# Optimization experiments

Measured on AMD Instinct MI355X. Metric: run time of the kernel, lower is better.

## Reference

```python
import jax, jax.numpy as jnp
import numpy as np

N_NODES = 30000
N_EDGES = 480000
N_GRAPHS = 64
NEG_SLOPE = 0.2
BN_EPS = 1e-5


def _leaky_relu(x, slope=NEG_SLOPE):
    return jnp.where(x >= 0, x, slope * x)


def gat_layer(x, src, dst, W, att_src, att_dst, bias, heads, ch, n_nodes):
    # x: [N, F_in]; W: [F_in, heads*ch]
    h = (x @ W).reshape(n_nodes, heads, ch)            # [N,H,C]
    a_s = jnp.sum(h * att_src, axis=-1)                # [N,H]
    a_d = jnp.sum(h * att_dst, axis=-1)                # [N,H]
    e = _leaky_relu(a_s[src] + a_d[dst])               # [E,H] per-edge logits
    # edge-softmax over incoming edges of each destination node
    m = jax.ops.segment_max(e, dst, num_segments=n_nodes)   # [N,H]
    ex = jnp.exp(e - m[dst])
    denom = jax.ops.segment_sum(ex, dst, num_segments=n_nodes)
    alpha = ex / denom[dst]                            # [E,H]
    msg = alpha[:, :, None] * h[src]                   # [E,H,C]
    out = jax.ops.segment_sum(msg, dst, num_segments=n_nodes)  # [N,H,C]
    return out.reshape(n_nodes, heads * ch) + bias


def setup_inputs() -> dict:
    key = jax.random.key(0)
    ks = jax.random.split(key, 16)
    x = jax.random.normal(ks[0], (N_NODES, 3), dtype=jnp.float32)
    edge_index = jax.random.randint(ks[1], (2, N_EDGES), 0, N_NODES, dtype=jnp.int64)
    batch = jnp.sort(jax.random.randint(ks[2], (N_NODES,), 0, N_GRAPHS, dtype=jnp.int64))

    def glorot(k, shape):
        fan = shape[0] + shape[-1]
        s = jnp.sqrt(6.0 / fan)
        return jax.random.uniform(k, shape, jnp.float32, -s, s)

    params = dict(
        W1=glorot(ks[3], (3, 8 * 64)),
        att_src1=glorot(ks[4], (8, 64)) * 0.1,
        att_dst1=glorot(ks[5], (8, 64)) * 0.1,
        b1=jnp.zeros((8 * 64,), jnp.float32),
        W2=glorot(ks[6], (8 * 64, 4 * 32)),
        att_src2=glorot(ks[7], (4, 32)) * 0.1,
        att_dst2=glorot(ks[8], (4, 32)) * 0.1,
        b2=jnp.zeros((4 * 32,), jnp.float32),
        Wfc=glorot(ks[9], (4 * 32, 32)),
        bfc=jnp.zeros((32,), jnp.float32),
        bn_gamma=jnp.ones((32,), jnp.float32),
        bn_beta=jnp.zeros((32,), jnp.float32),
        Wheat=glorot(ks[10], (32, 3)),
        bheat=jnp.zeros((3,), jnp.float32),
        Wdehyd=glorot(ks[11], (32, 2)),
        bdehyd=jnp.zeros((2,), jnp.float32),
    )
    return {"x": x, "edge_index": edge_index, "batch": batch, **params}


def reference(x, edge_index, batch, W1, att_src1, att_dst1, b1,
              W2, att_src2, att_dst2, b2, Wfc, bfc, bn_gamma, bn_beta,
              Wheat, bheat, Wdehyd, bdehyd):
    n = x.shape[0]
    # GATConv adds self-loops by default
    loops = jnp.arange(n, dtype=edge_index.dtype)
    src = jnp.concatenate([edge_index[0], loops])
    dst = jnp.concatenate([edge_index[1], loops])

    x1 = jax.nn.relu(gat_layer(x, src, dst, W1, att_src1, att_dst1, b1, 8, 64, n))   # [N,512]
    x2 = jax.nn.relu(gat_layer(x1, src, dst, W2, att_src2, att_dst2, b2, 4, 32, n))  # [N,128]
    h = x1[:, : x2.shape[1]] + x2                                                    # [N,128]

    # global_mean_pool over graph ids
    sums = jax.ops.segment_sum(h, batch, num_segments=N_GRAPHS)                      # [G,128]
    cnts = jax.ops.segment_sum(jnp.ones((n,), h.dtype), batch, num_segments=N_GRAPHS)
    pooled = sums / jnp.maximum(cnts, 1.0)[:, None]

    z = pooled @ Wfc + bfc                                                           # [G,32]
    mu = jnp.mean(z, axis=0)
    var = jnp.var(z, axis=0)
    z = bn_gamma * (z - mu) / jnp.sqrt(var + BN_EPS) + bn_beta
    z = jax.nn.relu(z)
    return (z @ Wheat + bheat, z @ Wdehyd + bdehyd)
```

## Files before the change

### kernel.cpp

```cpp
#include <hip/hip_runtime.h>
#include <math.h>


#define N_NODES 30000
#define N_GRAPHS 64

__global__ __launch_bounds__(256) void k_att1(
    const float* __restrict__ x, const float* __restrict__ W1,
    const float* __restrict__ asw, const float* __restrict__ adw,
    float* __restrict__ a_s, float* __restrict__ a_d, int n)
{
    __shared__ float Ps[24], Pd[24];
    int t = threadIdx.x;
    if (t < 48) {
        int which = t / 24;
        int idx = t - which * 24;
        int d = idx >> 3, h = idx & 7;
        const float* av = (which ? adw : asw) + h * 64;
        const float* wr = W1 + d * 512 + h * 64;
        float s = 0.f;
        #pragma unroll 8
        for (int c = 0; c < 64; ++c) s = fmaf(wr[c], av[c], s);
        (which ? Pd : Ps)[idx] = s;
    }
    __syncthreads();
    int node = blockIdx.x * 256 + t;
    if (node >= n) return;
    float x0 = x[node * 3 + 0];
    float x1v = x[node * 3 + 1];
    float x2v = x[node * 3 + 2];
    #pragma unroll
    for (int h = 0; h < 8; ++h) {
        a_s[node * 8 + h] = fmaf(x0, Ps[h], fmaf(x1v, Ps[8 + h], x2v * Ps[16 + h]));
        a_d[node * 8 + h] = fmaf(x0, Pd[h], fmaf(x1v, Pd[8 + h], x2v * Pd[16 + h]));
    }
}

__global__ void k_deg(const int* __restrict__ ei, int* __restrict__ deg,
                      int E0, int n)
{
    int e = blockIdx.x * blockDim.x + threadIdx.x;
    int Et = E0 + n;
    if (e >= Et) return;
    int dst = (e < E0) ? ei[E0 + e] : (e - E0);
    atomicAdd(&deg[dst], 1);
}

__global__ __launch_bounds__(1024) void k_scan(
    const int* __restrict__ deg, int* __restrict__ rowstart,
    int* __restrict__ cursor, int n)
{
    __shared__ int wsum[16];
    __shared__ int woff[17];
    __shared__ int carry_s;
    int tid = threadIdx.x, lane = tid & 63, wid = tid >> 6;
    if (tid == 0) carry_s = 0;
    __syncthreads();
    int nchunks = (n + 1023) >> 10;
    for (int c = 0; c < nchunks; ++c) {
        int i = (c << 10) + tid;
        int v = (i < n) ? deg[i] : 0;
        int s = v;
        #pragma unroll
        for (int off = 1; off < 64; off <<= 1) {
            int t = __shfl_up(s, off);
            if (lane >= off) s += t;
        }
        if (lane == 63) wsum[wid] = s;
        __syncthreads();
        if (wid == 0) {
            int ws = (lane < 16) ? wsum[lane] : 0;
            #pragma unroll
            for (int off = 1; off < 16; off <<= 1) {
                int t = __shfl_up(ws, off);
                if (lane >= off) ws += t;
            }
            if (lane < 16) woff[lane + 1] = ws;
            if (lane == 0) woff[0] = 0;
        }
        __syncthreads();
        int excl = carry_s + woff[wid] + s - v;
        if (i < n) { rowstart[i] = excl; cursor[i] = excl; }
        __syncthreads();
        if (tid == 0) carry_s += woff[16];
        __syncthreads();
    }
    if (tid == 0) rowstart[n] = carry_s;
}

__global__ void k_fill(const int* __restrict__ ei, int* __restrict__ cursor,
                       int* __restrict__ csr, int E0, int n)
{
    int e = blockIdx.x * blockDim.x + threadIdx.x;
    int Et = E0 + n;
    if (e >= Et) return;
    int src, dst;
    if (e < E0) { src = ei[e]; dst = ei[E0 + e]; }
    else        { src = e - E0; dst = e - E0; }
    int pos = atomicAdd(&cursor[dst], 1);
    csr[pos] = src;
}

__global__ __launch_bounds__(256) void k_gat1(
    const float* __restrict__ x, const float* __restrict__ W1,
    const float* __restrict__ a_s, const float* __restrict__ a_d,
    const int* __restrict__ rowstart, const int* __restrict__ csr,
    const float* __restrict__ bias, float* __restrict__ x1, int n)
{
    int lane = threadIdx.x & 63;
    int node = blockIdx.x * 4 + (threadIdx.x >> 6);
    if (node >= n) return;
    int rs = rowstart[node], re = rowstart[node + 1];
    int hd = lane >> 3;
    int slot = lane & 7;
    float adn = a_d[node * 8 + hd];

    float m = -1e30f, ssum = 0.f, S0 = 0.f, S1 = 0.f, S2 = 0.f;
    for (int i = rs + slot; i < re; i += 8) {
        int src = csr[i];
        float e = a_s[src * 8 + hd] + adn;
        e = (e >= 0.f) ? e : 0.2f * e;
        float x0 = x[src * 3 + 0];
        float x1v = x[src * 3 + 1];
        float x2v = x[src * 3 + 2];
        float mn = fmaxf(m, e);
        float sc = __expf(m - mn);
        float wgt = __expf(e - mn);
        ssum = fmaf(ssum, sc, wgt);
        S0 = fmaf(S0, sc, wgt * x0);
        S1 = fmaf(S1, sc, wgt * x1v);
        S2 = fmaf(S2, sc, wgt * x2v);
        m = mn;
    }
    #pragma unroll
    for (int off = 1; off < 8; off <<= 1) {
        float mo = __shfl_xor(m, off);
        float so = __shfl_xor(ssum, off);
        float t0 = __shfl_xor(S0, off);
        float t1 = __shfl_xor(S1, off);
        float t2 = __shfl_xor(S2, off);
        float mn = fmaxf(m, mo);
        float scA = __expf(m - mn);
        float scB = __expf(mo - mn);
        ssum = ssum * scA + so * scB;
        S0 = S0 * scA + t0 * scB;
        S1 = S1 * scA + t1 * scB;
        S2 = S2 * scA + t2 * scB;
        m = mn;
    }
    float inv = 1.f / ssum;
    S0 *= inv; S1 *= inv; S2 *= inv;

    const float4* w0p = (const float4*)(W1 + lane * 8);
    const float4* w1p = (const float4*)(W1 + 512 + lane * 8);
    const float4* w2p = (const float4*)(W1 + 1024 + lane * 8);
    const float4* bp  = (const float4*)(bias + lane * 8);
    float4* xp = (float4*)(x1 + (size_t)node * 512 + lane * 8);
    #pragma unroll
    for (int q = 0; q < 2; ++q) {
        float4 w0 = w0p[q], w1 = w1p[q], w2 = w2p[q], b = bp[q];
        float4 o;
        o.x = fmaxf(fmaf(S0, w0.x, fmaf(S1, w1.x, fmaf(S2, w2.x, b.x))), 0.f);
        o.y = fmaxf(fmaf(S0, w0.y, fmaf(S1, w1.y, fmaf(S2, w2.y, b.y))), 0.f);
        o.z = fmaxf(fmaf(S0, w0.z, fmaf(S1, w1.z, fmaf(S2, w2.z, b.z))), 0.f);
        o.w = fmaxf(fmaf(S0, w0.w, fmaf(S1, w1.w, fmaf(S2, w2.w, b.w))), 0.f);
        xp[q] = o;
    }
}

#define BM2 32
__global__ __launch_bounds__(256) void k_gemm2(
    const float* __restrict__ x1, const float* __restrict__ W2,
    const float* __restrict__ asw, const float* __restrict__ adw,
    float* __restrict__ h2, float* __restrict__ a_s2, float* __restrict__ a_d2,
    int n)
{
    int tid = threadIdx.x;
    int tr = tid >> 5;
    int tc = tid & 31;
    int bm = blockIdx.x * BM2;

    float acc[4][4];
    #pragma unroll
    for (int r = 0; r < 4; ++r)
        #pragma unroll
        for (int c = 0; c < 4; ++c) acc[r][c] = 0.f;

    const float* arow[4];
    #pragma unroll
    for (int r = 0; r < 4; ++r) {
        int row = bm + tr * 4 + r;
        row = row < n ? row : (n - 1);
        arow[r] = x1 + (size_t)row * 512;
    }
    const float* bcol = W2 + tc * 4;

    for (int k = 0; k < 512; k += 4) {
        float a_[4][4];
        #pragma unroll
        for (int r = 0; r < 4; ++r) {
            float4 av = *(const float4*)(arow[r] + k);
            a_[r][0] = av.x; a_[r][1] = av.y; a_[r][2] = av.z; a_[r][3] = av.w;
        }
        float b_[4][4];
        #pragma unroll
        for (int kk = 0; kk < 4; ++kk) {
            float4 bv = *(const float4*)(bcol + (size_t)(k + kk) * 128);
            b_[kk][0] = bv.x; b_[kk][1] = bv.y; b_[kk][2] = bv.z; b_[kk][3] = bv.w;
        }
        #pragma unroll
        for (int kk = 0; kk < 4; ++kk)
            #pragma unroll
            for (int r = 0; r < 4; ++r)
                #pragma unroll
                for (int c = 0; c < 4; ++c)
                    acc[r][c] = fmaf(a_[r][kk], b_[kk][c], acc[r][c]);
    }

    #pragma unroll
    for (int r = 0; r < 4; ++r) {
        int row = bm + tr * 4 + r;
        if (row < n) {
            float4 o;
            o.x = acc[r][0]; o.y = acc[r][1]; o.z = acc[r][2]; o.w = acc[r][3];
            *(float4*)(h2 + (size_t)row * 128 + tc * 4) = o;
        }
    }

    float4 ws = *(const float4*)(asw + tc * 4);
    float4 wd = *(const float4*)(adw + tc * 4);
    float ps[4], pd[4];
    #pragma unroll
    for (int r = 0; r < 4; ++r) {
        ps[r] = acc[r][0] * ws.x + acc[r][1] * ws.y + acc[r][2] * ws.z + acc[r][3] * ws.w;
        pd[r] = acc[r][0] * wd.x + acc[r][1] * wd.y + acc[r][2] * wd.z + acc[r][3] * wd.w;
    }
    #pragma unroll
    for (int off = 1; off < 8; off <<= 1) {
        #pragma unroll
        for (int r = 0; r < 4; ++r) {
            ps[r] += __shfl_xor(ps[r], off);
            pd[r] += __shfl_xor(pd[r], off);
        }
    }
    if ((tc & 7) == 0) {
        int hd = tc >> 3;
        #pragma unroll
        for (int r = 0; r < 4; ++r) {
            int row = bm + tr * 4 + r;
            if (row < n) {
                a_s2[row * 4 + hd] = ps[r];
                a_d2[row * 4 + hd] = pd[r];
            }
        }
    }
}

__global__ __launch_bounds__(256) void k_gat2(
    const float* __restrict__ h2, const float* __restrict__ a_s,
    const float* __restrict__ a_d, const int* __restrict__ rowstart,
    const int* __restrict__ csr, const float* __restrict__ bias,
    const float* __restrict__ x1, float* __restrict__ hres, int n)
{
    int lane = threadIdx.x & 63;
    int node = blockIdx.x * 4 + (threadIdx.x >> 6);
    if (node >= n) return;
    int rs = rowstart[node], re = rowstart[node + 1];
    int hd = lane >> 4;
    float adn = a_d[node * 4 + hd];

    float m = -1e30f, ssum = 0.f, acc0 = 0.f, acc1 = 0.f;
    int src_next = (rs < re) ? csr[rs] : 0;
    for (int i = rs; i < re; ++i) {
        int src = src_next;
        if (i + 1 < re) src_next = csr[i + 1];
        float e = a_s[src * 4 + hd] + adn;
        e = (e >= 0.f) ? e : 0.2f * e;
        float2 hv = *(const float2*)(h2 + (size_t)src * 128 + lane * 2);
        float mn = fmaxf(m, e);
        float sc = __expf(m - mn);
        float wgt = __expf(e - mn);
        ssum = fmaf(ssum, sc, wgt);
        acc0 = fmaf(acc0, sc, wgt * hv.x);
        acc1 = fmaf(acc1, sc, wgt * hv.y);
        m = mn;
    }
    float inv = 1.f / ssum;
    float2 xv = *(const float2*)(x1 + (size_t)node * 512 + lane * 2);
    float2 o;
    o.x = xv.x + fmaxf(fmaf(acc0, inv, bias[lane * 2 + 0]), 0.f);
    o.y = xv.y + fmaxf(fmaf(acc1, inv, bias[lane * 2 + 1]), 0.f);
    *(float2*)(hres + (size_t)node * 128 + lane * 2) = o;
}

__global__ __launch_bounds__(128) void k_pool(
    const float* __restrict__ hres, const int* __restrict__ batch,
    float* __restrict__ pooled, float* __restrict__ cnt, int n)
{
    int j = threadIdx.x;
    int n0 = blockIdx.x * 128;
    if (n0 >= n) return;
    int n1 = min(n0 + 128, n);
    int g = batch[n0];
    float acc = 0.f;
    int run = 0;
    for (int node = n0; node < n1; ++node) {
        int gb = batch[node];
        if (gb != g) {
            atomicAdd(&pooled[g * 128 + j], acc);
            if (j == 0) atomicAdd(&cnt[g], (float)run);
            acc = 0.f; run = 0; g = gb;
        }
        acc += hres[(size_t)node * 128 + j];
        run++;
    }
    atomicAdd(&pooled[g * 128 + j], acc);
    if (j == 0) atomicAdd(&cnt[g], (float)run);
}

__global__ __launch_bounds__(1024) void k_head(
    const float* __restrict__ pooled, const float* __restrict__ cnt,
    const float* __restrict__ Wfc, const float* __restrict__ bfc,
    const float* __restrict__ gamma, const float* __restrict__ beta,
    const float* __restrict__ Wheat, const float* __restrict__ bheat,
    const float* __restrict__ Wdehyd, const float* __restrict__ bdehyd,
    float* __restrict__ out)
{
    __shared__ float z[N_GRAPHS * 32];
    __shared__ float mu_s[32], rstd_s[32];
    int t = threadIdx.x;
    for (int idx = t; idx < N_GRAPHS * 32; idx += 1024) {
        int g = idx >> 5, j = idx & 31;
        float c = cnt[g];
        c = c < 1.f ? 1.f : c;
        float s = 0.f;
        for (int k = 0; k < 128; ++k)
            s = fmaf(pooled[g * 128 + k], Wfc[k * 32 + j], s);
        z[idx] = s / c + bfc[j];
    }
    __syncthreads();
    if (t < 32) {
        float mu = 0.f;
        for (int g = 0; g < N_GRAPHS; ++g) mu += z[g * 32 + t];
        mu *= (1.f / N_GRAPHS);
        float var = 0.f;
        for (int g = 0; g < N_GRAPHS; ++g) {
            float d = z[g * 32 + t] - mu;
            var = fmaf(d, d, var);
        }
        var *= (1.f / N_GRAPHS);
        mu_s[t] = mu;
        rstd_s[t] = 1.f / sqrtf(var + 1e-5f);
    }
    __syncthreads();
    for (int idx = t; idx < N_GRAPHS * 32; idx += 1024) {
        int j = idx & 31;
        float v = gamma[j] * (z[idx] - mu_s[j]) * rstd_s[j] + beta[j];
        z[idx] = v > 0.f ? v : 0.f;
    }
    __syncthreads();
    if (t < N_GRAPHS * 3) {
        int g = t / 3, r = t - g * 3;
        float s = 0.f;
        for (int j2 = 0; j2 < 32; ++j2)
            s = fmaf(z[g * 32 + j2], Wheat[j2 * 3 + r], s);
        out[t] = s + bheat[r];
    } else if (t < N_GRAPHS * 3 + N_GRAPHS * 2) {
        int idx = t - N_GRAPHS * 3;
        int g = idx >> 1, r = idx & 1;
        float s = 0.f;
        for (int j2 = 0; j2 < 32; ++j2)
            s = fmaf(z[g * 32 + j2], Wdehyd[j2 * 2 + r], s);
        out[N_GRAPHS * 3 + idx] = s + bdehyd[r];
    }
}

extern "C" void kernel_launch(void* const* d_in, const int* in_sizes, int n_in,
                              void* d_out, int out_size, void* d_ws, size_t ws_size,
                              hipStream_t stream)
{
    const float* x      = (const float*)d_in[0];
    const int*   ei     = (const int*)d_in[1];
    const int*   batch  = (const int*)d_in[2];
    const float* W1     = (const float*)d_in[3];
    const float* as1w   = (const float*)d_in[4];
    const float* ad1w   = (const float*)d_in[5];
    const float* b1     = (const float*)d_in[6];
    const float* W2     = (const float*)d_in[7];
    const float* as2w   = (const float*)d_in[8];
    const float* ad2w   = (const float*)d_in[9];
    const float* b2     = (const float*)d_in[10];
    const float* Wfc    = (const float*)d_in[11];
    const float* bfc    = (const float*)d_in[12];
    const float* gamma  = (const float*)d_in[13];
    const float* beta   = (const float*)d_in[14];
    const float* Wheat  = (const float*)d_in[15];
    const float* bheat  = (const float*)d_in[16];
    const float* Wdehyd = (const float*)d_in[17];
    const float* bdehyd = (const float*)d_in[18];
    float* out = (float*)d_out;

    const int N = N_NODES;
    const int E0 = in_sizes[1] / 2;
    const int Et = E0 + N;
    const int G = N_GRAPHS;

    char* w = (char*)d_ws;
    auto alloc = [&](size_t bytes) -> char* {
        char* p = w;
        w += (bytes + 255) & ~(size_t)255;
        return p;
    };
    float* x1    = (float*)alloc((size_t)N * 512 * 4);
    float* h2    = (float*)alloc((size_t)N * 128 * 4);
    float* hres  = (float*)alloc((size_t)N * 128 * 4);
    float* a_s1  = (float*)alloc((size_t)N * 8 * 4);
    float* a_d1  = (float*)alloc((size_t)N * 8 * 4);
    float* a_s2  = (float*)alloc((size_t)N * 4 * 4);
    float* a_d2  = (float*)alloc((size_t)N * 4 * 4);
    int* deg     = (int*)alloc((size_t)(N + 1) * 4);
    int* rowstart= (int*)alloc((size_t)(N + 1) * 4);
    int* cursor  = (int*)alloc((size_t)N * 4);
    int* csr     = (int*)alloc((size_t)Et * 4);
    float* pooled= (float*)alloc((size_t)G * 128 * 4);
    float* cntf  = (float*)alloc((size_t)G * 4);

    hipMemsetAsync(deg, 0, (size_t)(N + 1) * 4, stream);
    hipMemsetAsync(pooled, 0, (size_t)G * 128 * 4, stream);
    hipMemsetAsync(cntf, 0, (size_t)G * 4, stream);

    k_att1<<<(N + 255) / 256, 256, 0, stream>>>(x, W1, as1w, ad1w, a_s1, a_d1, N);
    k_deg<<<(Et + 255) / 256, 256, 0, stream>>>(ei, deg, E0, N);
    k_scan<<<1, 1024, 0, stream>>>(deg, rowstart, cursor, N);
    k_fill<<<(Et + 255) / 256, 256, 0, stream>>>(ei, cursor, csr, E0, N);
    k_gat1<<<(N + 3) / 4, 256, 0, stream>>>(x, W1, a_s1, a_d1, rowstart, csr, b1, x1, N);
    k_gemm2<<<(N + BM2 - 1) / BM2, 256, 0, stream>>>(x1, W2, as2w, ad2w, h2, a_s2, a_d2, N);
    k_gat2<<<(N + 3) / 4, 256, 0, stream>>>(h2, a_s2, a_d2, rowstart, csr, b2, x1, hres, N);
    k_pool<<<(N + 127) / 128, 128, 0, stream>>>(hres, batch, pooled, cntf, N);
    k_head<<<1, 1024, 0, stream>>>(pooled, cntf, Wfc, bfc, gamma, beta,
                                   Wheat, bheat, Wdehyd, bdehyd, out);
}
```

Measured before the change: 438.7 us.

## Tile layer-2 GEMM through double-buffered shared memory with larger per-thread blocks

The layer-2 projection GEMM, which used to read A and B straight from global memory per thread, now stages 64x32 A tiles (stored transposed and padded) and 32x128 W2 tiles in double-buffered LDS, prefetching the next tile into registers while computing. Each thread now computes a 4x8 output block instead of 4x4, and the attention-dot reductions are adjusted to the new column mapping. This is meant to cut redundant global/L2 traffic and raise arithmetic intensity, at the cost of more LDS use and registers, which can lower occupancy.

```diff
diff --git a/kernel.cpp b/kernel.cpp
--- a/kernel.cpp
+++ b/kernel.cpp
@@ -168,89 +168,164 @@
     }
 }
 
-#define BM2 32
+#define GM_BM 64
+#define GM_BK 32
+#define GM_APAD 68
 __global__ __launch_bounds__(256) void k_gemm2(
     const float* __restrict__ x1, const float* __restrict__ W2,
     const float* __restrict__ asw, const float* __restrict__ adw,
     float* __restrict__ h2, float* __restrict__ a_s2, float* __restrict__ a_d2,
     int n)
 {
+    __shared__ float As[2][GM_BK][GM_APAD];
+    __shared__ float Bs[2][GM_BK][128];
     int tid = threadIdx.x;
-    int tr = tid >> 5;
-    int tc = tid & 31;
-    int bm = blockIdx.x * BM2;
-
-    float acc[4][4];
+    int tr = tid >> 4;
+    int tc = tid & 15;
+    int bm = blockIdx.x * GM_BM;
+
+    int aRow0 = tid >> 3;
+    int aC40  = tid & 7;
+    int aRow1 = (tid + 256) >> 3;
+    int aC41  = (tid + 256) & 7;
+    float4 aReg0, aReg1, bReg[4];
+
+    int arowg0 = bm + aRow0; arowg0 = arowg0 < n ? arowg0 : (n - 1);
+    int arowg1 = bm + aRow1; arowg1 = arowg1 < n ? arowg1 : (n - 1);
+    const float* aPtr0 = x1 + (size_t)arowg0 * 512 + aC40 * 4;
+    const float* aPtr1 = x1 + (size_t)arowg1 * 512 + aC41 * 4;
+
+    float acc[4][8];
     #pragma unroll
     for (int r = 0; r < 4; ++r)
         #pragma unroll
-        for (int c = 0; c < 4; ++c) acc[r][c] = 0.f;
-
-    const float* arow[4];
-    #pragma unroll
-    for (int r = 0; r < 4; ++r) {
-        int row = bm + tr * 4 + r;
-        row = row < n ? row : (n - 1);
-        arow[r] = x1 + (size_t)row * 512;
-    }
-    const float* bcol = W2 + tc * 4;
-
-    for (int k = 0; k < 512; k += 4) {
-        float a_[4][4];
+        for (int c = 0; c < 8; ++c) acc[r][c] = 0.f;
+
+    {
+        aReg0 = *(const float4*)(aPtr0);
+        aReg1 = *(const float4*)(aPtr1);
         #pragma unroll
-        for (int r = 0; r < 4; ++r) {
-            float4 av = *(const float4*)(arow[r] + k);
-            a_[r][0] = av.x; a_[r][1] = av.y; a_[r][2] = av.z; a_[r][3] = av.w;
-        }
-        float b_[4][4];
+        for (int j = 0; j < 4; ++j) {
+            int li = tid + j * 256;
+            bReg[j] = *(const float4*)(W2 + (size_t)(li >> 5) * 128 + (li & 31) * 4);
+        }
+        As[0][aC40 * 4 + 0][aRow0] = aReg0.x;
+        As[0][aC40 * 4 + 1][aRow0] = aReg0.y;
+        As[0][aC40 * 4 + 2][aRow0] = aReg0.z;
+        As[0][aC40 * 4 + 3][aRow0] = aReg0.w;
+        As[0][aC41 * 4 + 0][aRow1] = aReg1.x;
+        As[0][aC41 * 4 + 1][aRow1] = aReg1.y;
+        As[0][aC41 * 4 + 2][aRow1] = aReg1.z;
+        As[0][aC41 * 4 + 3][aRow1] = aReg1.w;
         #pragma unroll
-        for (int kk = 0; kk < 4; ++kk) {
-            float4 bv = *(const float4*)(bcol + (size_t)(k + kk) * 128);
-            b_[kk][0] = bv.x; b_[kk][1] = bv.y; b_[kk][2] = bv.z; b_[kk][3] = bv.w;
+        for (int j = 0; j < 4; ++j) {
+            int li = tid + j * 256;
+            *(float4*)(&Bs[0][li >> 5][(li & 31) * 4]) = bReg[j];
+        }
+    }
+    __syncthreads();
+
+    for (int s = 0; s < 16; ++s) {
+        int buf = s & 1;
+        if (s < 15) {
+            int k0 = (s + 1) * GM_BK;
+            aReg0 = *(const float4*)(aPtr0 + k0);
+            aReg1 = *(const float4*)(aPtr1 + k0);
+            #pragma unroll
+            for (int j = 0; j < 4; ++j) {
+                int li = tid + j * 256;
+                bReg[j] = *(const float4*)(W2 + (size_t)(k0 + (li >> 5)) * 128 + (li & 31) * 4);
+            }
         }
         #pragma unroll
-        for (int kk = 0; kk < 4; ++kk)
+        for (int kk = 0; kk < GM_BK; ++kk) {
+            float4 a4 = *(const float4*)(&As[buf][kk][tr * 4]);
+            float4 b0 = *(const float4*)(&Bs[buf][kk][tc * 8]);
+            float4 b1 = *(const float4*)(&Bs[buf][kk][tc * 8 + 4]);
+            acc[0][0] = fmaf(a4.x, b0.x, acc[0][0]);
+            acc[0][1] = fmaf(a4.x, b0.y, acc[0][1]);
+            acc[0][2] = fmaf(a4.x, b0.z, acc[0][2]);
+            acc[0][3] = fmaf(a4.x, b0.w, acc[0][3]);
+            acc[0][4] = fmaf(a4.x, b1.x, acc[0][4]);
+            acc[0][5] = fmaf(a4.x, b1.y, acc[0][5]);
+            acc[0][6] = fmaf(a4.x, b1.z, acc[0][6]);
+            acc[0][7] = fmaf(a4.x, b1.w, acc[0][7]);
+            acc[1][0] = fmaf(a4.y, b0.x, acc[1][0]);
+            acc[1][1] = fmaf(a4.y, b0.y, acc[1][1]);
+            acc[1][2] = fmaf(a4.y, b0.z, acc[1][2]);
+            acc[1][3] = fmaf(a4.y, b0.w, acc[1][3]);
+            acc[1][4] = fmaf(a4.y, b1.x, acc[1][4]);
+            acc[1][5] = fmaf(a4.y, b1.y, acc[1][5]);
+            acc[1][6] = fmaf(a4.y, b1.z, acc[1][6]);
+            acc[1][7] = fmaf(a4.y, b1.w, acc[1][7]);
+            acc[2][0] = fmaf(a4.z, b0.x, acc[2][0]);
+            acc[2][1] = fmaf(a4.z, b0.y, acc[2][1]);
+            acc[2][2] = fmaf(a4.z, b0.z, acc[2][2]);
+            acc[2][3] = fmaf(a4.z, b0.w, acc[2][3]);
+            acc[2][4] = fmaf(a4.z, b1.x, acc[2][4]);
+            acc[2][5] = fmaf(a4.z, b1.y, acc[2][5]);
+            acc[2][6] = fmaf(a4.z, b1.z, acc[2][6]);
+            acc[2][7] = fmaf(a4.z, b1.w, acc[2][7]);
+            acc[3][0] = fmaf(a4.w, b0.x, acc[3][0]);
+            acc[3][1] = fmaf(a4.w, b0.y, acc[3][1]);
+            acc[3][2] = fmaf(a4.w, b0.z, acc[3][2]);
+            acc[3][3] = fmaf(a4.w, b0.w, acc[3][3]);
+            acc[3][4] = fmaf(a4.w, b1.x, acc[3][4]);
+            acc[3][5] = fmaf(a4.w, b1.y, acc[3][5]);
+            acc[3][6] = fmaf(a4.w, b1.z, acc[3][6]);
+            acc[3][7] = fmaf(a4.w, b1.w, acc[3][7]);
+        }
+        if (s < 15) {
+            int nb = buf ^ 1;
+            As[nb][aC40 * 4 + 0][aRow0] = aReg0.x;
+            As[nb][aC40 * 4 + 1][aRow0] = aReg0.y;
+            As[nb][aC40 * 4 + 2][aRow0] = aReg0.z;
+            As[nb][aC40 * 4 + 3][aRow0] = aReg0.w;
+            As[nb][aC41 * 4 + 0][aRow1] = aReg1.x;
+            As[nb][aC41 * 4 + 1][aRow1] = aReg1.y;
+            As[nb][aC41 * 4 + 2][aRow1] = aReg1.z;
+            As[nb][aC41 * 4 + 3][aRow1] = aReg1.w;
             #pragma unroll
-            for (int r = 0; r < 4; ++r)
-                #pragma unroll
-                for (int c = 0; c < 4; ++c)
-                    acc[r][c] = fmaf(a_[r][kk], b_[kk][c], acc[r][c]);
+            for (int j = 0; j < 4; ++j) {
+                int li = tid + j * 256;
+                *(float4*)(&Bs[nb][li >> 5][(li & 31) * 4]) = bReg[j];
+            }
+            __syncthreads();
+        }
     }
 
     #pragma unroll
     for (int r = 0; r < 4; ++r) {
         int row = bm + tr * 4 + r;
         if (row < n) {
-            float4 o;
-            o.x = acc[r][0]; o.y = acc[r][1]; o.z = acc[r][2]; o.w = acc[r][3];
-            *(float4*)(h2 + (size_t)row * 128 + tc * 4) = o;
-        }
-    }
-
-    float4 ws = *(const float4*)(asw + tc * 4);
-    float4 wd = *(const float4*)(adw + tc * 4);
-    float ps[4], pd[4];
+            float4 o0, o1;
+            o0.x = acc[r][0]; o0.y = acc[r][1]; o0.z = acc[r][2]; o0.w = acc[r][3];
+            o1.x = acc[r][4]; o1.y = acc[r][5]; o1.z = acc[r][6]; o1.w = acc[r][7];
+            *(float4*)(h2 + (size_t)row * 128 + tc * 8) = o0;
+            *(float4*)(h2 + (size_t)row * 128 + tc * 8 + 4) = o1;
+        }
+    }
+
+    float4 ws0 = *(const float4*)(asw + tc * 8);
+    float4 ws1 = *(const float4*)(asw + tc * 8 + 4);
+    float4 wd0 = *(const float4*)(adw + tc * 8);
+    float4 wd1 = *(const float4*)(adw + tc * 8 + 4);
     #pragma unroll
     for (int r = 0; r < 4; ++r) {
-        ps[r] = acc[r][0] * ws.x + acc[r][1] * ws.y + acc[r][2] * ws.z + acc[r][3] * ws.w;
-        pd[r] = acc[r][0] * wd.x + acc[r][1] * wd.y + acc[r][2] * wd.z + acc[r][3] * wd.w;
-    }
-    #pragma unroll
-    for (int off = 1; off < 8; off <<= 1) {
-        #pragma unroll
-        for (int r = 0; r < 4; ++r) {
-            ps[r] += __shfl_xor(ps[r], off);
-            pd[r] += __shfl_xor(pd[r], off);
-        }
-    }
-    if ((tc & 7) == 0) {
-        int hd = tc >> 3;
-        #pragma unroll
-        for (int r = 0; r < 4; ++r) {
+        float ps = acc[r][0] * ws0.x + acc[r][1] * ws0.y + acc[r][2] * ws0.z +
+                   acc[r][3] * ws0.w + acc[r][4] * ws1.x + acc[r][5] * ws1.y +
+                   acc[r][6] * ws1.z + acc[r][7] * ws1.w;
+        float pd = acc[r][0] * wd0.x + acc[r][1] * wd0.y + acc[r][2] * wd0.z +
+                   acc[r][3] * wd0.w + acc[r][4] * wd1.x + acc[r][5] * wd1.y +
+                   acc[r][6] * wd1.z + acc[r][7] * wd1.w;
+        ps += __shfl_xor(ps, 1); ps += __shfl_xor(ps, 2);
+        pd += __shfl_xor(pd, 1); pd += __shfl_xor(pd, 2);
+        if ((tc & 3) == 0) {
             int row = bm + tr * 4 + r;
             if (row < n) {
-                a_s2[row * 4 + hd] = ps[r];
-                a_d2[row * 4 + hd] = pd[r];
+                int hd = tc >> 2;
+                a_s2[row * 4 + hd] = ps;
+                a_d2[row * 4 + hd] = pd;
             }
         }
     }
@@ -434,7 +509,7 @@
     k_scan<<<1, 1024, 0, stream>>>(deg, rowstart, cursor, N);
     k_fill<<<(Et + 255) / 256, 256, 0, stream>>>(ei, cursor, csr, E0, N);
     k_gat1<<<(N + 3) / 4, 256, 0, stream>>>(x, W1, a_s1, a_d1, rowstart, csr, b1, x1, N);
-    k_gemm2<<<(N + BM2 - 1) / BM2, 256, 0, stream>>>(x1, W2, as2w, ad2w, h2, a_s2, a_d2, N);
+    k_gemm2<<<(N + GM_BM - 1) / GM_BM, 256, 0, stream>>>(x1, W2, as2w, ad2w, h2, a_s2, a_d2, N);
     k_gat2<<<(N + 3) / 4, 256, 0, stream>>>(h2, a_s2, a_d2, rowstart, csr, b2, x1, hres, N);
     k_pool<<<(N + 127) / 128, 128, 0, stream>>>(hres, batch, pooled, cntf, N);
     k_head<<<1, 1024, 0, stream>>>(pooled, cntf, Wfc, bfc, gamma, beta,
```

New measurement: 427.1 us. 1.03x faster.

## Stop materialising x1; recompute from per-head aggregates inside GEMM and GAT2

Applied to the files above, without the earlier changes.

Layer 1 only writes per-node, per-head normalised aggregates of the 3-wide input (a 32-float Shat) instead of the 512-wide x1. The second-layer GEMM rebuilds each x1 tile on the fly from Shat, W1 and bias before ReLU, and the residual in gat2 does the same recomputation. The GEMM itself becomes an LDS-tiled, double-buffered 64x128 kernel with a 4x8 register tile. This removes writing and rereading roughly 60MB of x1 traffic, at the cost of some extra FMAs and shared memory use.

```diff
diff --git a/kernel.cpp b/kernel.cpp
--- a/kernel.cpp
+++ b/kernel.cpp
@@ -102,10 +102,9 @@
 }
 
 __global__ __launch_bounds__(256) void k_gat1(
-    const float* __restrict__ x, const float* __restrict__ W1,
-    const float* __restrict__ a_s, const float* __restrict__ a_d,
-    const int* __restrict__ rowstart, const int* __restrict__ csr,
-    const float* __restrict__ bias, float* __restrict__ x1, int n)
+    const float* __restrict__ x, const float* __restrict__ a_s,
+    const float* __restrict__ a_d, const int* __restrict__ rowstart,
+    const int* __restrict__ csr, float* __restrict__ Shat, int n)
 {
     int lane = threadIdx.x & 63;
     int node = blockIdx.x * 4 + (threadIdx.x >> 6);
@@ -148,109 +147,167 @@
         S2 = S2 * scA + t2 * scB;
         m = mn;
     }
-    float inv = 1.f / ssum;
-    S0 *= inv; S1 *= inv; S2 *= inv;
-
-    const float4* w0p = (const float4*)(W1 + lane * 8);
-    const float4* w1p = (const float4*)(W1 + 512 + lane * 8);
-    const float4* w2p = (const float4*)(W1 + 1024 + lane * 8);
-    const float4* bp  = (const float4*)(bias + lane * 8);
-    float4* xp = (float4*)(x1 + (size_t)node * 512 + lane * 8);
-    #pragma unroll
-    for (int q = 0; q < 2; ++q) {
-        float4 w0 = w0p[q], w1 = w1p[q], w2 = w2p[q], b = bp[q];
+    if (slot == 0) {
+        float inv = 1.f / ssum;
         float4 o;
-        o.x = fmaxf(fmaf(S0, w0.x, fmaf(S1, w1.x, fmaf(S2, w2.x, b.x))), 0.f);
-        o.y = fmaxf(fmaf(S0, w0.y, fmaf(S1, w1.y, fmaf(S2, w2.y, b.y))), 0.f);
-        o.z = fmaxf(fmaf(S0, w0.z, fmaf(S1, w1.z, fmaf(S2, w2.z, b.z))), 0.f);
-        o.w = fmaxf(fmaf(S0, w0.w, fmaf(S1, w1.w, fmaf(S2, w2.w, b.w))), 0.f);
-        xp[q] = o;
-    }
-}
-
-#define BM2 32
+        o.x = S0 * inv; o.y = S1 * inv; o.z = S2 * inv; o.w = 0.f;
+        *(float4*)(Shat + ((size_t)node * 8 + hd) * 4) = o;
+    }
+}
+
+#define GM_BM 64
+#define GM_BK 32
+#define GM_APAD 68
 __global__ __launch_bounds__(256) void k_gemm2(
-    const float* __restrict__ x1, const float* __restrict__ W2,
+    const float* __restrict__ Shat, const float* __restrict__ W1,
+    const float* __restrict__ bias1, const float* __restrict__ W2,
     const float* __restrict__ asw, const float* __restrict__ adw,
     float* __restrict__ h2, float* __restrict__ a_s2, float* __restrict__ a_d2,
     int n)
 {
+    __shared__ float As[2][GM_BK][GM_APAD];
+    __shared__ float Bs[2][GM_BK][128];
     int tid = threadIdx.x;
-    int tr = tid >> 5;
-    int tc = tid & 31;
-    int bm = blockIdx.x * BM2;
-
-    float acc[4][4];
+    int tr = tid >> 4;
+    int tc = tid & 15;
+    int bm = blockIdx.x * GM_BM;
+
+    int sRow = tid & 63;
+    int sKq  = (tid >> 6) << 3;
+    int srowg = bm + sRow; if (srowg >= n) srowg = n - 1;
+    const float* shp = Shat + (size_t)srowg * 32;
+
+    float acc[4][8];
     #pragma unroll
     for (int r = 0; r < 4; ++r)
         #pragma unroll
-        for (int c = 0; c < 4; ++c) acc[r][c] = 0.f;
-
-    const float* arow[4];
-    #pragma unroll
-    for (int r = 0; r < 4; ++r) {
-        int row = bm + tr * 4 + r;
-        row = row < n ? row : (n - 1);
-        arow[r] = x1 + (size_t)row * 512;
-    }
-    const float* bcol = W2 + tc * 4;
-
-    for (int k = 0; k < 512; k += 4) {
-        float a_[4][4];
-        #pragma unroll
-        for (int r = 0; r < 4; ++r) {
-            float4 av = *(const float4*)(arow[r] + k);
-            a_[r][0] = av.x; a_[r][1] = av.y; a_[r][2] = av.z; a_[r][3] = av.w;
-        }
-        float b_[4][4];
-        #pragma unroll
-        for (int kk = 0; kk < 4; ++kk) {
-            float4 bv = *(const float4*)(bcol + (size_t)(k + kk) * 128);
-            b_[kk][0] = bv.x; b_[kk][1] = bv.y; b_[kk][2] = bv.z; b_[kk][3] = bv.w;
-        }
-        #pragma unroll
-        for (int kk = 0; kk < 4; ++kk)
-            #pragma unroll
-            for (int r = 0; r < 4; ++r)
-                #pragma unroll
-                for (int c = 0; c < 4; ++c)
-                    acc[r][c] = fmaf(a_[r][kk], b_[kk][c], acc[r][c]);
+        for (int c = 0; c < 8; ++c) acc[r][c] = 0.f;
+
+    float4 sh, wA0, wA1, wB0, wB1, wC0, wC1, bb0, bb1, bReg[4];
+
+    auto loadStage = [&](int s) {
+        int k0 = s * GM_BK;
+        sh  = *(const float4*)(shp + ((k0 >> 6) << 2));
+        const float* wk = W1 + k0 + sKq;
+        wA0 = *(const float4*)(wk);         wA1 = *(const float4*)(wk + 4);
+        wB0 = *(const float4*)(wk + 512);   wB1 = *(const float4*)(wk + 516);
+        wC0 = *(const float4*)(wk + 1024);  wC1 = *(const float4*)(wk + 1028);
+        bb0 = *(const float4*)(bias1 + k0 + sKq);
+        bb1 = *(const float4*)(bias1 + k0 + sKq + 4);
+        #pragma unroll
+        for (int j = 0; j < 4; ++j) {
+            int li = tid + j * 256;
+            bReg[j] = *(const float4*)(W2 + (size_t)(k0 + (li >> 5)) * 128 + (li & 31) * 4);
+        }
+    };
+    auto storeStage = [&](int b) {
+        float va[8];
+        va[0] = fmaf(sh.x, wA0.x, fmaf(sh.y, wB0.x, fmaf(sh.z, wC0.x, bb0.x)));
+        va[1] = fmaf(sh.x, wA0.y, fmaf(sh.y, wB0.y, fmaf(sh.z, wC0.y, bb0.y)));
+        va[2] = fmaf(sh.x, wA0.z, fmaf(sh.y, wB0.z, fmaf(sh.z, wC0.z, bb0.z)));
+        va[3] = fmaf(sh.x, wA0.w, fmaf(sh.y, wB0.w, fmaf(sh.z, wC0.w, bb0.w)));
+        va[4] = fmaf(sh.x, wA1.x, fmaf(sh.y, wB1.x, fmaf(sh.z, wC1.x, bb1.x)));
+        va[5] = fmaf(sh.x, wA1.y, fmaf(sh.y, wB1.y, fmaf(sh.z, wC1.y, bb1.y)));
+        va[6] = fmaf(sh.x, wA1.z, fmaf(sh.y, wB1.z, fmaf(sh.z, wC1.z, bb1.z)));
+        va[7] = fmaf(sh.x, wA1.w, fmaf(sh.y, wB1.w, fmaf(sh.z, wC1.w, bb1.w)));
+        #pragma unroll
+        for (int j = 0; j < 8; ++j)
+            As[b][sKq + j][sRow] = fmaxf(va[j], 0.f);
+        #pragma unroll
+        for (int j = 0; j < 4; ++j) {
+            int li = tid + j * 256;
+            *(float4*)(&Bs[b][li >> 5][(li & 31) * 4]) = bReg[j];
+        }
+    };
+
+    loadStage(0);
+    storeStage(0);
+    __syncthreads();
+
+    for (int s = 0; s < 16; ++s) {
+        int buf = s & 1;
+        if (s < 15) loadStage(s + 1);
+        #pragma unroll
+        for (int kk = 0; kk < GM_BK; ++kk) {
+            float4 a4  = *(const float4*)(&As[buf][kk][tr * 4]);
+            float4 b0  = *(const float4*)(&Bs[buf][kk][tc * 4]);
+            float4 b1v = *(const float4*)(&Bs[buf][kk][64 + tc * 4]);
+            acc[0][0] = fmaf(a4.x, b0.x, acc[0][0]);
+            acc[0][1] = fmaf(a4.x, b0.y, acc[0][1]);
+            acc[0][2] = fmaf(a4.x, b0.z, acc[0][2]);
+            acc[0][3] = fmaf(a4.x, b0.w, acc[0][3]);
+            acc[0][4] = fmaf(a4.x, b1v.x, acc[0][4]);
+            acc[0][5] = fmaf(a4.x, b1v.y, acc[0][5]);
+            acc[0][6] = fmaf(a4.x, b1v.z, acc[0][6]);
+            acc[0][7] = fmaf(a4.x, b1v.w, acc[0][7]);
+            acc[1][0] = fmaf(a4.y, b0.x, acc[1][0]);
+            acc[1][1] = fmaf(a4.y, b0.y, acc[1][1]);
+            acc[1][2] = fmaf(a4.y, b0.z, acc[1][2]);
+            acc[1][3] = fmaf(a4.y, b0.w, acc[1][3]);
+            acc[1][4] = fmaf(a4.y, b1v.x, acc[1][4]);
+            acc[1][5] = fmaf(a4.y, b1v.y, acc[1][5]);
+            acc[1][6] = fmaf(a4.y, b1v.z, acc[1][6]);
+            acc[1][7] = fmaf(a4.y, b1v.w, acc[1][7]);
+            acc[2][0] = fmaf(a4.z, b0.x, acc[2][0]);
+            acc[2][1] = fmaf(a4.z, b0.y, acc[2][1]);
+            acc[2][2] = fmaf(a4.z, b0.z, acc[2][2]);
+            acc[2][3] = fmaf(a4.z, b0.w, acc[2][3]);
+            acc[2][4] = fmaf(a4.z, b1v.x, acc[2][4]);
+            acc[2][5] = fmaf(a4.z, b1v.y, acc[2][5]);
+            acc[2][6] = fmaf(a4.z, b1v.z, acc[2][6]);
+            acc[2][7] = fmaf(a4.z, b1v.w, acc[2][7]);
+            acc[3][0] = fmaf(a4.w, b0.x, acc[3][0]);
+            acc[3][1] = fmaf(a4.w, b0.y, acc[3][1]);
+            acc[3][2] = fmaf(a4.w, b0.z, acc[3][2]);
+            acc[3][3] = fmaf(a4.w, b0.w, acc[3][3]);
+            acc[3][4] = fmaf(a4.w, b1v.x, acc[3][4]);
+            acc[3][5] = fmaf(a4.w, b1v.y, acc[3][5]);
+            acc[3][6] = fmaf(a4.w, b1v.z, acc[3][6]);
+            acc[3][7] = fmaf(a4.w, b1v.w, acc[3][7]);
+        }
+        if (s < 15) {
+            storeStage(buf ^ 1);
+            __syncthreads();
+        }
     }
 
     #pragma unroll
     for (int r = 0; r < 4; ++r) {
         int row = bm + tr * 4 + r;
         if (row < n) {
-            float4 o;
-            o.x = acc[r][0]; o.y = acc[r][1]; o.z = acc[r][2]; o.w = acc[r][3];
-            *(float4*)(h2 + (size_t)row * 128 + tc * 4) = o;
-        }
-    }
-
-    float4 ws = *(const float4*)(asw + tc * 4);
-    float4 wd = *(const float4*)(adw + tc * 4);
-    float ps[4], pd[4];
+            float4 oL, oH;
+            oL.x = acc[r][0]; oL.y = acc[r][1]; oL.z = acc[r][2]; oL.w = acc[r][3];
+            oH.x = acc[r][4]; oH.y = acc[r][5]; oH.z = acc[r][6]; oH.w = acc[r][7];
+            *(float4*)(h2 + (size_t)row * 128 + tc * 4) = oL;
+            *(float4*)(h2 + (size_t)row * 128 + 64 + tc * 4) = oH;
+        }
+    }
+
+    float4 wsL = *(const float4*)(asw + tc * 4);
+    float4 wsH = *(const float4*)(asw + 64 + tc * 4);
+    float4 wdL = *(const float4*)(adw + tc * 4);
+    float4 wdH = *(const float4*)(adw + 64 + tc * 4);
     #pragma unroll
     for (int r = 0; r < 4; ++r) {
-        ps[r] = acc[r][0] * ws.x + acc[r][1] * ws.y + acc[r][2] * ws.z + acc[r][3] * ws.w;
-        pd[r] = acc[r][0] * wd.x + acc[r][1] * wd.y + acc[r][2] * wd.z + acc[r][3] * wd.w;
-    }
-    #pragma unroll
-    for (int off = 1; off < 8; off <<= 1) {
-        #pragma unroll
-        for (int r = 0; r < 4; ++r) {
-            ps[r] += __shfl_xor(ps[r], off);
-            pd[r] += __shfl_xor(pd[r], off);
-        }
-    }
-    if ((tc & 7) == 0) {
-        int hd = tc >> 3;
-        #pragma unroll
-        for (int r = 0; r < 4; ++r) {
+        float psL = acc[r][0] * wsL.x + acc[r][1] * wsL.y + acc[r][2] * wsL.z + acc[r][3] * wsL.w;
+        float pdL = acc[r][0] * wdL.x + acc[r][1] * wdL.y + acc[r][2] * wdL.z + acc[r][3] * wdL.w;
+        float psH = acc[r][4] * wsH.x + acc[r][5] * wsH.y + acc[r][6] * wsH.z + acc[r][7] * wsH.w;
+        float pdH = acc[r][4] * wdH.x + acc[r][5] * wdH.y + acc[r][6] * wdH.z + acc[r][7] * wdH.w;
+        #pragma unroll
+        for (int off = 1; off < 8; off <<= 1) {
+            psL += __shfl_xor(psL, off);
+            pdL += __shfl_xor(pdL, off);
+            psH += __shfl_xor(psH, off);
+            pdH += __shfl_xor(pdH, off);
+        }
+        if ((tc & 7) == 0) {
             int row = bm + tr * 4 + r;
             if (row < n) {
-                a_s2[row * 4 + hd] = ps[r];
-                a_d2[row * 4 + hd] = pd[r];
+                int h0 = tc >> 3;
+                a_s2[row * 4 + h0] = psL;
+                a_d2[row * 4 + h0] = pdL;
+                a_s2[row * 4 + 2 + h0] = psH;
+                a_d2[row * 4 + 2 + h0] = pdH;
             }
         }
     }
@@ -260,7 +317,8 @@
     const float* __restrict__ h2, const float* __restrict__ a_s,
     const float* __restrict__ a_d, const int* __restrict__ rowstart,
     const int* __restrict__ csr, const float* __restrict__ bias,
-    const float* __restrict__ x1, float* __restrict__ hres, int n)
+    const float* __restrict__ Shat, const float* __restrict__ W1,
+    const float* __restrict__ bias1, float* __restrict__ hres, int n)
 {
     int lane = threadIdx.x & 63;
     int node = blockIdx.x * 4 + (threadIdx.x >> 6);
@@ -286,10 +344,19 @@
         m = mn;
     }
     float inv = 1.f / ssum;
-    float2 xv = *(const float2*)(x1 + (size_t)node * 512 + lane * 2);
+
+    int hh = lane >> 5;
+    float4 shv = *(const float4*)(Shat + ((size_t)node * 8 + hh) * 4);
+    float2 w0 = *(const float2*)(W1 + lane * 2);
+    float2 w1v = *(const float2*)(W1 + 512 + lane * 2);
+    float2 w2v = *(const float2*)(W1 + 1024 + lane * 2);
+    float2 bv = *(const float2*)(bias1 + lane * 2);
+    float r0 = fmaxf(fmaf(shv.x, w0.x, fmaf(shv.y, w1v.x, fmaf(shv.z, w2v.x, bv.x))), 0.f);
+    float r1 = fmaxf(fmaf(shv.x, w0.y, fmaf(shv.y, w1v.y, fmaf(shv.z, w2v.y, bv.y))), 0.f);
+
     float2 o;
-    o.x = xv.x + fmaxf(fmaf(acc0, inv, bias[lane * 2 + 0]), 0.f);
-    o.y = xv.y + fmaxf(fmaf(acc1, inv, bias[lane * 2 + 1]), 0.f);
+    o.x = r0 + fmaxf(fmaf(acc0, inv, bias[lane * 2 + 0]), 0.f);
+    o.y = r1 + fmaxf(fmaf(acc1, inv, bias[lane * 2 + 1]), 0.f);
     *(float2*)(hres + (size_t)node * 128 + lane * 2) = o;
 }
 
@@ -411,7 +478,7 @@
         w += (bytes + 255) & ~(size_t)255;
         return p;
     };
-    float* x1    = (float*)alloc((size_t)N * 512 * 4);
+    float* Shat  = (float*)alloc((size_t)N * 32 * 4);
     float* h2    = (float*)alloc((size_t)N * 128 * 4);
     float* hres  = (float*)alloc((size_t)N * 128 * 4);
     float* a_s1  = (float*)alloc((size_t)N * 8 * 4);
@@ -433,9 +500,9 @@
     k_deg<<<(Et + 255) / 256, 256, 0, stream>>>(ei, deg, E0, N);
     k_scan<<<1, 1024, 0, stream>>>(deg, rowstart, cursor, N);
     k_fill<<<(Et + 255) / 256, 256, 0, stream>>>(ei, cursor, csr, E0, N);
-    k_gat1<<<(N + 3) / 4, 256, 0, stream>>>(x, W1, a_s1, a_d1, rowstart, csr, b1, x1, N);
-    k_gemm2<<<(N + BM2 - 1) / BM2, 256, 0, stream>>>(x1, W2, as2w, ad2w, h2, a_s2, a_d2, N);
-    k_gat2<<<(N + 3) / 4, 256, 0, stream>>>(h2, a_s2, a_d2, rowstart, csr, b2, x1, hres, N);
+    k_gat1<<<(N + 3) / 4, 256, 0, stream>>>(x, a_s1, a_d1, rowstart, csr, Shat, N);
+    k_gemm2<<<(N + GM_BM - 1) / GM_BM, 256, 0, stream>>>(Shat, W1, b1, W2, as2w, ad2w, h2, a_s2, a_d2, N);
+    k_gat2<<<(N + 3) / 4, 256, 0, stream>>>(h2, a_s2, a_d2, rowstart, csr, b2, Shat, W1, b1, hres, N);
     k_pool<<<(N + 127) / 128, 128, 0, stream>>>(hres, batch, pooled, cntf, N);
     k_head<<<1, 1024, 0, stream>>>(pooled, cntf, Wfc, bfc, gamma, beta,
                                    Wheat, bheat, Wdehyd, bdehyd, out);
```

After: 419.1 us. -4.5%, faster.

## Store compact aggregated inputs instead of x1 and recompute layer-1 output on the fly

Applied to the files above, without the earlier changes.

Layer 1 now writes only the normalized aggregated 3-dim input per node and head (32 floats per node) instead of the full 512-wide x1 activation. The layer-2 GEMM rebuilds x1 tiles in shared memory from that compact form plus W1 and the bias. The residual in gat2 rebuilds its slice the same way. The GEMM also gains shared-memory tiling for A and B. This removes about 60 MB of global writes and reads of x1, at the cost of redundant recompute FMAs and extra syncthreads.

```diff
diff --git a/kernel.cpp b/kernel.cpp
--- a/kernel.cpp
+++ b/kernel.cpp
@@ -102,10 +102,9 @@
 }
 
 __global__ __launch_bounds__(256) void k_gat1(
-    const float* __restrict__ x, const float* __restrict__ W1,
-    const float* __restrict__ a_s, const float* __restrict__ a_d,
-    const int* __restrict__ rowstart, const int* __restrict__ csr,
-    const float* __restrict__ bias, float* __restrict__ x1, int n)
+    const float* __restrict__ x, const float* __restrict__ a_s,
+    const float* __restrict__ a_d, const int* __restrict__ rowstart,
+    const int* __restrict__ csr, float* __restrict__ Shat, int n)
 {
     int lane = threadIdx.x & 63;
     int node = blockIdx.x * 4 + (threadIdx.x >> 6);
@@ -148,37 +147,35 @@
         S2 = S2 * scA + t2 * scB;
         m = mn;
     }
-    float inv = 1.f / ssum;
-    S0 *= inv; S1 *= inv; S2 *= inv;
-
-    const float4* w0p = (const float4*)(W1 + lane * 8);
-    const float4* w1p = (const float4*)(W1 + 512 + lane * 8);
-    const float4* w2p = (const float4*)(W1 + 1024 + lane * 8);
-    const float4* bp  = (const float4*)(bias + lane * 8);
-    float4* xp = (float4*)(x1 + (size_t)node * 512 + lane * 8);
-    #pragma unroll
-    for (int q = 0; q < 2; ++q) {
-        float4 w0 = w0p[q], w1 = w1p[q], w2 = w2p[q], b = bp[q];
+    if (slot == 0) {
+        float inv = 1.f / ssum;
         float4 o;
-        o.x = fmaxf(fmaf(S0, w0.x, fmaf(S1, w1.x, fmaf(S2, w2.x, b.x))), 0.f);
-        o.y = fmaxf(fmaf(S0, w0.y, fmaf(S1, w1.y, fmaf(S2, w2.y, b.y))), 0.f);
-        o.z = fmaxf(fmaf(S0, w0.z, fmaf(S1, w1.z, fmaf(S2, w2.z, b.z))), 0.f);
-        o.w = fmaxf(fmaf(S0, w0.w, fmaf(S1, w1.w, fmaf(S2, w2.w, b.w))), 0.f);
-        xp[q] = o;
-    }
-}
-
-#define BM2 32
+        o.x = S0 * inv; o.y = S1 * inv; o.z = S2 * inv; o.w = 0.f;
+        *(float4*)(Shat + ((size_t)node * 8 + hd) * 4) = o;
+    }
+}
+
+#define GM_BM 32
+#define GM_BK 32
+#define GM_APAD 36
 __global__ __launch_bounds__(256) void k_gemm2(
-    const float* __restrict__ x1, const float* __restrict__ W2,
+    const float* __restrict__ Shat, const float* __restrict__ W1,
+    const float* __restrict__ bias1, const float* __restrict__ W2,
     const float* __restrict__ asw, const float* __restrict__ adw,
     float* __restrict__ h2, float* __restrict__ a_s2, float* __restrict__ a_d2,
     int n)
 {
+    __shared__ float As[GM_BK][GM_APAD];
+    __shared__ float Bs[GM_BK][128];
     int tid = threadIdx.x;
     int tr = tid >> 5;
     int tc = tid & 31;
-    int bm = blockIdx.x * BM2;
+    int bm = blockIdx.x * GM_BM;
+
+    int sRow = tid & 31;
+    int sK4  = (tid >> 5) << 2;
+    int srowg = bm + sRow; if (srowg >= n) srowg = n - 1;
+    const float* shp = Shat + (size_t)srowg * 32;
 
     float acc[4][4];
     #pragma unroll
@@ -186,35 +183,49 @@
         #pragma unroll
         for (int c = 0; c < 4; ++c) acc[r][c] = 0.f;
 
-    const float* arow[4];
-    #pragma unroll
-    for (int r = 0; r < 4; ++r) {
-        int row = bm + tr * 4 + r;
-        row = row < n ? row : (n - 1);
-        arow[r] = x1 + (size_t)row * 512;
-    }
-    const float* bcol = W2 + tc * 4;
-
-    for (int k = 0; k < 512; k += 4) {
-        float a_[4][4];
+    for (int s = 0; s < 16; ++s) {
+        int k0 = s * GM_BK;
+        {
+            int kg = k0 + sK4;
+            float4 sh = *(const float4*)(shp + ((kg >> 6) << 2));
+            float4 w0 = *(const float4*)(W1 + kg);
+            float4 w1v = *(const float4*)(W1 + 512 + kg);
+            float4 w2v = *(const float4*)(W1 + 1024 + kg);
+            float4 bb = *(const float4*)(bias1 + kg);
+            As[sK4 + 0][sRow] = fmaxf(fmaf(sh.x, w0.x, fmaf(sh.y, w1v.x, fmaf(sh.z, w2v.x, bb.x))), 0.f);
+            As[sK4 + 1][sRow] = fmaxf(fmaf(sh.x, w0.y, fmaf(sh.y, w1v.y, fmaf(sh.z, w2v.y, bb.y))), 0.f);
+            As[sK4 + 2][sRow] = fmaxf(fmaf(sh.x, w0.z, fmaf(sh.y, w1v.z, fmaf(sh.z, w2v.z, bb.z))), 0.f);
+            As[sK4 + 3][sRow] = fmaxf(fmaf(sh.x, w0.w, fmaf(sh.y, w1v.w, fmaf(sh.z, w2v.w, bb.w))), 0.f);
+        }
         #pragma unroll
-        for (int r = 0; r < 4; ++r) {
-            float4 av = *(const float4*)(arow[r] + k);
-            a_[r][0] = av.x; a_[r][1] = av.y; a_[r][2] = av.z; a_[r][3] = av.w;
-        }
-        float b_[4][4];
+        for (int j = 0; j < 4; ++j) {
+            int li = tid + j * 256;
+            *(float4*)(&Bs[li >> 5][(li & 31) * 4]) =
+                *(const float4*)(W2 + (size_t)(k0 + (li >> 5)) * 128 + (li & 31) * 4);
+        }
+        __syncthreads();
         #pragma unroll
-        for (int kk = 0; kk < 4; ++kk) {
-            float4 bv = *(const float4*)(bcol + (size_t)(k + kk) * 128);
-            b_[kk][0] = bv.x; b_[kk][1] = bv.y; b_[kk][2] = bv.z; b_[kk][3] = bv.w;
-        }
-        #pragma unroll
-        for (int kk = 0; kk < 4; ++kk)
-            #pragma unroll
-            for (int r = 0; r < 4; ++r)
-                #pragma unroll
-                for (int c = 0; c < 4; ++c)
-                    acc[r][c] = fmaf(a_[r][kk], b_[kk][c], acc[r][c]);
+        for (int kk = 0; kk < GM_BK; ++kk) {
+            float4 a4 = *(const float4*)(&As[kk][tr * 4]);
+            float4 b4 = *(const float4*)(&Bs[kk][tc * 4]);
+            acc[0][0] = fmaf(a4.x, b4.x, acc[0][0]);
+            acc[0][1] = fmaf(a4.x, b4.y, acc[0][1]);
+            acc[0][2] = fmaf(a4.x, b4.z, acc[0][2]);
+            acc[0][3] = fmaf(a4.x, b4.w, acc[0][3]);
+            acc[1][0] = fmaf(a4.y, b4.x, acc[1][0]);
+            acc[1][1] = fmaf(a4.y, b4.y, acc[1][1]);
+            acc[1][2] = fmaf(a4.y, b4.z, acc[1][2]);
+            acc[1][3] = fmaf(a4.y, b4.w, acc[1][3]);
+            acc[2][0] = fmaf(a4.z, b4.x, acc[2][0]);
+            acc[2][1] = fmaf(a4.z, b4.y, acc[2][1]);
+            acc[2][2] = fmaf(a4.z, b4.z, acc[2][2]);
+            acc[2][3] = fmaf(a4.z, b4.w, acc[2][3]);
+            acc[3][0] = fmaf(a4.w, b4.x, acc[3][0]);
+            acc[3][1] = fmaf(a4.w, b4.y, acc[3][1]);
+            acc[3][2] = fmaf(a4.w, b4.z, acc[3][2]);
+            acc[3][3] = fmaf(a4.w, b4.w, acc[3][3]);
+        }
+        if (s < 15) __syncthreads();
     }
 
     #pragma unroll
@@ -229,28 +240,18 @@
 
     float4 ws = *(const float4*)(asw + tc * 4);
     float4 wd = *(const float4*)(adw + tc * 4);
-    float ps[4], pd[4];
     #pragma unroll
     for (int r = 0; r < 4; ++r) {
-        ps[r] = acc[r][0] * ws.x + acc[r][1] * ws.y + acc[r][2] * ws.z + acc[r][3] * ws.w;
-        pd[r] = acc[r][0] * wd.x + acc[r][1] * wd.y + acc[r][2] * wd.z + acc[r][3] * wd.w;
-    }
-    #pragma unroll
-    for (int off = 1; off < 8; off <<= 1) {
-        #pragma unroll
-        for (int r = 0; r < 4; ++r) {
-            ps[r] += __shfl_xor(ps[r], off);
-            pd[r] += __shfl_xor(pd[r], off);
-        }
-    }
-    if ((tc & 7) == 0) {
-        int hd = tc >> 3;
-        #pragma unroll
-        for (int r = 0; r < 4; ++r) {
+        float ps = acc[r][0] * ws.x + acc[r][1] * ws.y + acc[r][2] * ws.z + acc[r][3] * ws.w;
+        float pd = acc[r][0] * wd.x + acc[r][1] * wd.y + acc[r][2] * wd.z + acc[r][3] * wd.w;
+        ps += __shfl_xor(ps, 1); ps += __shfl_xor(ps, 2); ps += __shfl_xor(ps, 4);
+        pd += __shfl_xor(pd, 1); pd += __shfl_xor(pd, 2); pd += __shfl_xor(pd, 4);
+        if ((tc & 7) == 0) {
             int row = bm + tr * 4 + r;
             if (row < n) {
-                a_s2[row * 4 + hd] = ps[r];
-                a_d2[row * 4 + hd] = pd[r];
+                int hd = tc >> 3;
+                a_s2[row * 4 + hd] = ps;
+                a_d2[row * 4 + hd] = pd;
             }
         }
     }
@@ -260,7 +261,8 @@
     const float* __restrict__ h2, const float* __restrict__ a_s,
     const float* __restrict__ a_d, const int* __restrict__ rowstart,
     const int* __restrict__ csr, const float* __restrict__ bias,
-    const float* __restrict__ x1, float* __restrict__ hres, int n)
+    const float* __restrict__ Shat, const float* __restrict__ W1,
+    const float* __restrict__ bias1, float* __restrict__ hres, int n)
 {
     int lane = threadIdx.x & 63;
     int node = blockIdx.x * 4 + (threadIdx.x >> 6);
@@ -286,10 +288,19 @@
         m = mn;
     }
     float inv = 1.f / ssum;
-    float2 xv = *(const float2*)(x1 + (size_t)node * 512 + lane * 2);
+
+    int hh = lane >> 5;
+    float4 shv = *(const float4*)(Shat + ((size_t)node * 8 + hh) * 4);
+    float2 w0 = *(const float2*)(W1 + lane * 2);
+    float2 w1v = *(const float2*)(W1 + 512 + lane * 2);
+    float2 w2v = *(const float2*)(W1 + 1024 + lane * 2);
+    float2 bv = *(const float2*)(bias1 + lane * 2);
+    float r0 = fmaxf(fmaf(shv.x, w0.x, fmaf(shv.y, w1v.x, fmaf(shv.z, w2v.x, bv.x))), 0.f);
+    float r1 = fmaxf(fmaf(shv.x, w0.y, fmaf(shv.y, w1v.y, fmaf(shv.z, w2v.y, bv.y))), 0.f);
+
     float2 o;
-    o.x = xv.x + fmaxf(fmaf(acc0, inv, bias[lane * 2 + 0]), 0.f);
-    o.y = xv.y + fmaxf(fmaf(acc1, inv, bias[lane * 2 + 1]), 0.f);
+    o.x = r0 + fmaxf(fmaf(acc0, inv, bias[lane * 2 + 0]), 0.f);
+    o.y = r1 + fmaxf(fmaf(acc1, inv, bias[lane * 2 + 1]), 0.f);
     *(float2*)(hres + (size_t)node * 128 + lane * 2) = o;
 }
 
@@ -411,7 +422,7 @@
         w += (bytes + 255) & ~(size_t)255;
         return p;
     };
-    float* x1    = (float*)alloc((size_t)N * 512 * 4);
+    float* Shat  = (float*)alloc((size_t)N * 32 * 4);
     float* h2    = (float*)alloc((size_t)N * 128 * 4);
     float* hres  = (float*)alloc((size_t)N * 128 * 4);
     float* a_s1  = (float*)alloc((size_t)N * 8 * 4);
@@ -433,9 +444,9 @@
     k_deg<<<(Et + 255) / 256, 256, 0, stream>>>(ei, deg, E0, N);
     k_scan<<<1, 1024, 0, stream>>>(deg, rowstart, cursor, N);
     k_fill<<<(Et + 255) / 256, 256, 0, stream>>>(ei, cursor, csr, E0, N);
-    k_gat1<<<(N + 3) / 4, 256, 0, stream>>>(x, W1, a_s1, a_d1, rowstart, csr, b1, x1, N);
-    k_gemm2<<<(N + BM2 - 1) / BM2, 256, 0, stream>>>(x1, W2, as2w, ad2w, h2, a_s2, a_d2, N);
-    k_gat2<<<(N + 3) / 4, 256, 0, stream>>>(h2, a_s2, a_d2, rowstart, csr, b2, x1, hres, N);
+    k_gat1<<<(N + 3) / 4, 256, 0, stream>>>(x, a_s1, a_d1, rowstart, csr, Shat, N);
+    k_gemm2<<<(N + GM_BM - 1) / GM_BM, 256, 0, stream>>>(Shat, W1, b1, W2, as2w, ad2w, h2, a_s2, a_d2, N);
+    k_gat2<<<(N + 3) / 4, 256, 0, stream>>>(h2, a_s2, a_d2, rowstart, csr, b2, Shat, W1, b1, hres, N);
     k_pool<<<(N + 127) / 128, 128, 0, stream>>>(hres, batch, pooled, cntf, N);
     k_head<<<1, 1024, 0, stream>>>(pooled, cntf, Wfc, bfc, gamma, beta,
                                    Wheat, bheat, Wdehyd, bdehyd, out);
```

Result: faster. 415.4 us (-5.3%).
